# Performance work log

Hardware: AMD Instinct MI355X
Metric: run time of the kernel (lower is better)

## Reference

```python
import jax, jax.numpy as jnp
import numpy as np

B, D_IN, HD, HN = 16384, 1024, 128, 8
D = HD * HN  # 1024
PROJ = int((4.0 / 3.0) * D)  # 1365
EPS = 1e-5


def setup_inputs() -> dict:
    key = jax.random.key(0)
    ks = jax.random.split(key, 16)
    s = 0.02
    inp = {
        'seq': jax.random.normal(ks[0], (B, D_IN), jnp.float32),
        'c0': jnp.zeros((B, D), jnp.float32),
        'n0': jnp.ones((B, D), jnp.float32),
        'h0': jax.random.normal(ks[1], (B, D), jnp.float32) * 0.1,
        'm0': jnp.zeros((B, D), jnp.float32),
        'ln_w': jnp.ones((D_IN,), jnp.float32),
        'ln_b': jnp.zeros((D_IN,), jnp.float32),
        'Wz': jax.random.normal(ks[2], (D, D_IN), jnp.float32) * s,
        'bz': jnp.zeros((D,), jnp.float32),
        'Wi': jax.random.normal(ks[3], (D, D_IN), jnp.float32) * s,
        'bi': jnp.zeros((D,), jnp.float32),
        'Wo': jax.random.normal(ks[4], (D, D_IN), jnp.float32) * s,
        'bo': jnp.zeros((D,), jnp.float32),
        'Wf': jax.random.normal(ks[5], (D, D_IN), jnp.float32) * s,
        'bf': jnp.zeros((D,), jnp.float32),
        'Rz': jax.random.normal(ks[6], (HN, HD, HD), jnp.float32) * s,
        'Ri': jax.random.normal(ks[7], (HN, HD, HD), jnp.float32) * s,
        'Ro': jax.random.normal(ks[8], (HN, HD, HD), jnp.float32) * s,
        'Rf': jax.random.normal(ks[9], (HN, HD, HD), jnp.float32) * s,
        'gn_w': jnp.ones((D,), jnp.float32),
        'gn_b': jnp.zeros((D,), jnp.float32),
        'up_w': jax.random.normal(ks[10], (2 * PROJ, D), jnp.float32) * s,
        'up_b': jnp.zeros((2 * PROJ,), jnp.float32),
        'down_w': jax.random.normal(ks[11], (D_IN, PROJ), jnp.float32) * s,
        'down_b': jnp.zeros((D_IN,), jnp.float32),
    }
    return inp


def _layernorm(x, w, b):
    mu = jnp.mean(x, axis=-1, keepdims=True)
    var = jnp.mean(jnp.square(x - mu), axis=-1, keepdims=True)
    return (x - mu) * jax.lax.rsqrt(var + EPS) * w + b


def _groupnorm(x, w, b):
    # x: (B, D) -> groups of HD channels per head
    xr = x.reshape(x.shape[0], HN, HD)
    mu = jnp.mean(xr, axis=-1, keepdims=True)
    var = jnp.mean(jnp.square(xr - mu), axis=-1, keepdims=True)
    xn = ((xr - mu) * jax.lax.rsqrt(var + EPS)).reshape(x.shape)
    return xn * w + b


def _block_linear(h, R):
    # block-diagonal recurrence: per-head (HD,HD) matmul
    hr = h.reshape(h.shape[0], HN, HD)
    return jnp.einsum('hed,bhd->bhe', R, hr).reshape(h.shape)


def reference(seq, c0, n0, h0, m0, ln_w, ln_b, Wz, bz, Wi, bi, Wo, bo, Wf, bf,
              Rz, Ri, Ro, Rf, gn_w, gn_b, up_w, up_b, down_w, down_b):
    x_t = _layernorm(seq, ln_w, ln_b)
    x_c = x_t  # use_conv=False default path
    i_t = x_c @ Wi.T + bi + _block_linear(h0, Ri)
    f_t = x_c @ Wf.T + bf + _block_linear(h0, Rf)
    z_t = x_t @ Wz.T + bz + _block_linear(h0, Rz)
    o_t = x_t @ Wo.T + bo + _block_linear(h0, Ro)
    m_t = jnp.maximum(f_t + m0, i_t)
    i_e = jnp.exp(i_t - m_t)
    f_e = jnp.exp(f_t - m_t + m0)
    z_a = jnp.tanh(z_t)
    o_a = jax.nn.sigmoid(o_t)
    c_t = f_e * c0 + i_e * z_a
    n_t = f_e * n0 + i_e
    h_t = o_a * (c_t / n_t)
    out = _groupnorm(h_t, gn_w, gn_b)
    up = out @ up_w.T + up_b
    out1, out2 = jnp.split(up, 2, axis=-1)
    out = out1 + jax.nn.gelu(out2, approximate=False)
    out = out @ down_w.T + down_b
    return (out + seq, c_t, n_t, h_t, m_t)
```

## Files before the change

### kernel.cpp

```cpp
#include <hip/hip_runtime.h>
#include <hip/hip_bf16.h>
#include <cstdint>
#include <type_traits>

typedef __attribute__((ext_vector_type(8))) __bf16 bf16x8;
typedef __attribute__((ext_vector_type(8))) short short8;
typedef __attribute__((ext_vector_type(4))) float f32x4;
using u16 = unsigned short;

template <typename T, typename = void> struct mfma_ok : std::false_type {};
template <typename T>
struct mfma_ok<T, std::void_t<decltype(__builtin_amdgcn_mfma_f32_16x16x32_bf16(
    std::declval<T>(), std::declval<T>(), std::declval<f32x4>(), 0, 0, 0))>>
    : std::true_type {};
using frag_t = std::conditional_t<mfma_ok<bf16x8>::value, bf16x8, short8>;
static_assert(sizeof(frag_t) == 16, "frag must be 4 VGPRs");

template <typename T>
__device__ __forceinline__ f32x4 MFMA(T a, T b, f32x4 c) {
  return __builtin_amdgcn_mfma_f32_16x16x32_bf16(a, b, c, 0, 0, 0);
}

__device__ __forceinline__ void gl_lds16(const u16* g, u16* l) {
  __builtin_amdgcn_global_load_lds(
      (const __attribute__((address_space(1))) unsigned int*)g,
      (__attribute__((address_space(3))) unsigned int*)l, 16, 0, 0);
}

__device__ __forceinline__ u16 f2bf(float v) {
  __hip_bfloat16 h = __float2bfloat16(v);
  return __builtin_bit_cast(u16, h);
}

__device__ __forceinline__ int xcd_swz(int wid, int nwg) {
  return (wid & 7) * (nwg >> 3) + (wid >> 3);
}

__device__ __forceinline__ void gemm256(
    const u16* __restrict__ A, int lda,
    const u16* __restrict__ B, int ldb, int K,
    u16* lds, f32x4 (&acc)[8][4])
{
  const int t = threadIdx.x;
  const int l = t & 63;
  const int w = t >> 6;
  const int wm = w >> 2, wc = w & 3;

  const int sr = t >> 2;
  const int cs = (t & 3) ^ ((sr & 3) ^ ((sr >> 2) & 3));
  const u16* gA = A + sr * lda + cs * 8;
  const u16* gB = B + sr * ldb + cs * 8;

  const int lr = l & 15;
  const int kceff = (l >> 4) ^ ((l & 3) ^ ((l >> 2) & 3));
  const int abase = wm * 4096 + lr * 32 + kceff * 8;
  const int bbase = 8192 + wc * 2048 + lr * 32 + kceff * 8;

  const int nt = K >> 5;

#define STG(buf, kt) do {                                      \
    u16* s_ = (buf);                                           \
    const u16* a_ = gA + (kt) * 32;                            \
    const u16* b_ = gB + (kt) * 32;                            \
    gl_lds16(a_,             s_ + w * 512);                    \
    gl_lds16(a_ + 128 * lda, s_ +  4096 + w * 512);            \
    gl_lds16(b_,             s_ +  8192 + w * 512);            \
    gl_lds16(b_ + 128 * ldb, s_ + 12288 + w * 512);            \
  } while (0)

  STG(lds, 0);
  asm volatile("s_waitcnt vmcnt(0)" ::: "memory");
  __builtin_amdgcn_s_barrier();

  for (int kt = 0; kt < nt; ++kt) {
    u16* cur = lds + (kt & 1) * 16384;
    u16* nxt = lds + ((kt + 1) & 1) * 16384;
    const bool more = (kt + 1 < nt);
    if (more) STG(nxt, kt + 1);

    frag_t a[8], b[4];
#pragma unroll
    for (int fm = 0; fm < 8; ++fm)
      a[fm] = *(const frag_t*)(cur + abase + fm * 512);
#pragma unroll
    for (int fn = 0; fn < 4; ++fn)
      b[fn] = *(const frag_t*)(cur + bbase + fn * 512);

    __builtin_amdgcn_s_setprio(1);
#pragma unroll
    for (int fn = 0; fn < 4; ++fn)
#pragma unroll
      for (int fm = 0; fm < 8; ++fm)
        acc[fm][fn] = MFMA(a[fm], b[fn], acc[fm][fn]);
    __builtin_amdgcn_s_setprio(0);

    if (more) asm volatile("s_waitcnt vmcnt(0)" ::: "memory");
    else      asm volatile("" ::: "memory");
    __builtin_amdgcn_s_barrier();
  }
#undef STG
}

__global__ __launch_bounds__(256) void prep_kernel(
    const float* __restrict__ Wi, const float* __restrict__ Wf,
    const float* __restrict__ Wz, const float* __restrict__ Wo,
    const float* __restrict__ Ri, const float* __restrict__ Rf,
    const float* __restrict__ Rz, const float* __restrict__ Ro,
    const float* __restrict__ upw, const float* __restrict__ dnw,
    u16* __restrict__ Wint, u16* __restrict__ Rint,
    u16* __restrict__ upint, u16* __restrict__ dnp)
{
  const int stride = gridDim.x * 256;
  for (int i = blockIdx.x * 256 + threadIdx.x; i < 9043968; i += stride) {
    if (i < 4194304) {
      const int s = i >> 18, v = (i >> 10) & 255, k = i & 1023;
      const int wc = v >> 6, gsel = (v >> 4) & 3, c16 = v & 15;
      const int srcRow = s * 64 + wc * 16 + c16;
      const float* W = (gsel == 0) ? Wi : (gsel == 1) ? Wf : (gsel == 2) ? Wz : Wo;
      Wint[i] = f2bf(W[srcRow * 1024 + k]);
    } else if (i < 4718592) {
      const int j = i - 4194304;
      const int s = j >> 15, v = (j >> 7) & 255, k = j & 127;
      const int wc = v >> 6, gsel = (v >> 4) & 3, c16 = v & 15;
      const int head = s >> 1;
      const int colInHead = (s & 1) * 64 + wc * 16 + c16;
      const float* R = (gsel == 0) ? Ri : (gsel == 1) ? Rf : (gsel == 2) ? Rz : Ro;
      Rint[j] = f2bf(R[head * 16384 + colInHead * 128 + k]);
    } else if (i < 7602176) {
      const int j = i - 4718592;
      const int vcol = j >> 10, k = j & 1023;
      const int tile = vcol >> 8, wc = (vcol >> 6) & 3;
      const int half = (vcol >> 5) & 1, c32 = vcol & 31;
      const int a = tile * 128 + wc * 32 + c32;
      upint[j] = (a < 1365) ? f2bf(upw[(half * 1365 + a) * 1024 + k]) : (u16)0;
    } else {
      const int j = i - 7602176;
      const int row = j / 1408, k = j - row * 1408;
      dnp[j] = (k < 1365) ? f2bf(dnw[row * 1365 + k]) : (u16)0;
    }
  }
}

__global__ __launch_bounds__(256) void ln_kernel(
    const float* __restrict__ seq, const float* __restrict__ h0,
    const float* __restrict__ lnw, const float* __restrict__ lnb,
    u16* __restrict__ xb, u16* __restrict__ h0b)
{
  const int row = blockIdx.x;
  const int t = threadIdx.x;
  const float4 v = ((const float4*)(seq + (size_t)row * 1024))[t];
  float s = v.x + v.y + v.z + v.w;
  float q = v.x * v.x + v.y * v.y + v.z * v.z + v.w * v.w;
#pragma unroll
  for (int o = 32; o >= 1; o >>= 1) { s += __shfl_xor(s, o); q += __shfl_xor(q, o); }
  __shared__ float sm[8];
  const int l = t & 63, w = t >> 6;
  if (l == 0) { sm[w] = s; sm[4 + w] = q; }
  __syncthreads();
  s = sm[0] + sm[1] + sm[2] + sm[3];
  q = sm[4] + sm[5] + sm[6] + sm[7];
  const float mu = s * (1.f / 1024.f);
  const float var = q * (1.f / 1024.f) - mu * mu;
  const float rstd = rsqrtf(var + 1e-5f);
  const float4 wv = ((const float4*)lnw)[t];
  const float4 bv = ((const float4*)lnb)[t];
  ushort4 o4;
  o4.x = f2bf((v.x - mu) * rstd * wv.x + bv.x);
  o4.y = f2bf((v.y - mu) * rstd * wv.y + bv.y);
  o4.z = f2bf((v.z - mu) * rstd * wv.z + bv.z);
  o4.w = f2bf((v.w - mu) * rstd * wv.w + bv.w);
  ((ushort4*)(xb + (size_t)row * 1024))[t] = o4;
  const float4 h = ((const float4*)(h0 + (size_t)row * 1024))[t];
  ushort4 h4;
  h4.x = f2bf(h.x); h4.y = f2bf(h.y); h4.z = f2bf(h.z); h4.w = f2bf(h.w);
  ((ushort4*)(h0b + (size_t)row * 1024))[t] = h4;
}

__global__ __launch_bounds__(512, 2) void gate_kernel(
    const u16* __restrict__ xb, const u16* __restrict__ h0b,
    const u16* __restrict__ Wint, const u16* __restrict__ Rint,
    const float* __restrict__ bi, const float* __restrict__ bfv,
    const float* __restrict__ bz, const float* __restrict__ bo,
    const float* __restrict__ c0, const float* __restrict__ n0i,
    const float* __restrict__ m0,
    float* __restrict__ oc, float* __restrict__ on,
    float* __restrict__ oh, float* __restrict__ om)
{
  __shared__ __align__(16) u16 lds[32768];
  const int wid = xcd_swz(blockIdx.x, 1024);
  const int s = wid & 15;
  const int m0r = (wid >> 4) * 256;
  f32x4 acc[8][4] = {};
  gemm256(xb + (size_t)m0r * 1024, 1024, Wint + s * 262144, 1024, 1024, lds, acc);
  const int head = s >> 1;
  gemm256(h0b + (size_t)m0r * 1024 + head * 128, 1024,
          Rint + s * 32768, 128, 128, lds, acc);

  const int t = threadIdx.x, l = t & 63, w = t >> 6, wm = w >> 2, wc = w & 3;
  const int cc = s * 64 + wc * 16 + (l & 15);
  const float biv = bi[cc], bfvv = bfv[cc], bzv = bz[cc], bov = bo[cc];
#pragma unroll
  for (int fm = 0; fm < 8; ++fm) {
    const int rbase = m0r + wm * 128 + fm * 16 + (l >> 4) * 4;
#pragma unroll
    for (int r = 0; r < 4; ++r) {
      const size_t idx = (size_t)(rbase + r) * 1024 + cc;
      const float it = acc[fm][0][r] + biv;
      const float ft = acc[fm][1][r] + bfvv;
      const float zt = acc[fm][2][r] + bzv;
      const float ot = acc[fm][3][r] + bov;
      const float mp = m0[idx];
      const float mt = fmaxf(ft + mp, it);
      const float ie = __expf(it - mt);
      const float fe = __expf(ft - mt + mp);
      const float ct = fe * c0[idx] + ie * tanhf(zt);
      const float nt = fe * n0i[idx] + ie;
      const float ht = (ct / nt) / (1.f + __expf(-ot));
      oc[idx] = ct; on[idx] = nt; oh[idx] = ht; om[idx] = mt;
    }
  }
}

__global__ __launch_bounds__(256) void gn_kernel(
    const float* __restrict__ h, const float* __restrict__ gw,
    const float* __restrict__ gb, u16* __restrict__ gnb)
{
  const int t = threadIdx.x, l = t & 63, w = t >> 6;
  for (int grp = blockIdx.x * 4 + w; grp < 16384 * 8; grp += gridDim.x * 4) {
    const int b = grp >> 3, hd = grp & 7;
    const float2 v = ((const float2*)(h + b * 1024 + hd * 128))[l];
    float s = v.x + v.y, q = v.x * v.x + v.y * v.y;
#pragma unroll
    for (int o = 32; o >= 1; o >>= 1) { s += __shfl_xor(s, o); q += __shfl_xor(q, o); }
    const float mu = s * (1.f / 128.f);
    const float var = q * (1.f / 128.f) - mu * mu;
    const float rstd = rsqrtf(var + 1e-5f);
    const float2 wv = ((const float2*)(gw + hd * 128))[l];
    const float2 bv = ((const float2*)(gb + hd * 128))[l];
    ushort2 o2;
    o2.x = f2bf((v.x - mu) * rstd * wv.x + bv.x);
    o2.y = f2bf((v.y - mu) * rstd * wv.y + bv.y);
    ((ushort2*)(gnb + b * 1024 + hd * 128))[l] = o2;
  }
}

__global__ __launch_bounds__(512, 2) void up_kernel(
    const u16* __restrict__ gnb, const u16* __restrict__ upint,
    const float* __restrict__ upb, u16* __restrict__ g)
{
  __shared__ __align__(16) u16 lds[32768];
  const int wid = xcd_swz(blockIdx.x, 704);
  const int vt = wid % 11, mt = wid / 11;
  const int m0r = mt * 256;
  f32x4 acc[8][4] = {};
  gemm256(gnb + (size_t)m0r * 1024, 1024, upint + vt * 262144, 1024, 1024,
          lds, acc);
  const int t = threadIdx.x, l = t & 63, w = t >> 6, wm = w >> 2, wc = w & 3;
#pragma unroll
  for (int fm = 0; fm < 8; ++fm) {
    const int rbase = m0r + wm * 128 + fm * 16 + (l >> 4) * 4;
#pragma unroll
    for (int fn = 0; fn < 2; ++fn) {
      const int a = vt * 128 + wc * 32 + fn * 16 + (l & 15);
      const float b1 = (a < 1365) ? upb[a] : 0.f;
      const float b2 = (a < 1365) ? upb[1365 + a] : 0.f;
#pragma unroll
      for (int r = 0; r < 4; ++r) {
        const float u1 = acc[fm][fn][r] + b1;
        const float u2 = acc[fm][fn + 2][r] + b2;
        const float ge = 0.5f * u2 * (1.f + erff(u2 * 0.70710678118654752f));
        g[(size_t)(rbase + r) * 1408 + a] = f2bf(u1 + ge);
      }
    }
  }
}

__global__ __launch_bounds__(512, 2) void down_kernel(
    const u16* __restrict__ g, const u16* __restrict__ dnp,
    const float* __restrict__ dnb, const float* __restrict__ seq,
    float* __restrict__ out)
{
  __shared__ __align__(16) u16 lds[32768];
  const int wid = xcd_swz(blockIdx.x, 256);
  const int nc = (wid & 3) * 256;
  const int m0r = (wid >> 2) * 256;
  f32x4 acc[8][4] = {};
  gemm256(g + (size_t)m0r * 1408, 1408, dnp + nc * 1408, 1408, 1408, lds, acc);
  const int t = threadIdx.x, l = t & 63, w = t >> 6, wm = w >> 2, wc = w & 3;
#pragma unroll
  for (int fm = 0; fm < 8; ++fm) {
    const int rbase = m0r + wm * 128 + fm * 16 + (l >> 4) * 4;
#pragma unroll
    for (int fn = 0; fn < 4; ++fn) {
      const int cc = nc + wc * 64 + fn * 16 + (l & 15);
      const float bb = dnb[cc];
#pragma unroll
      for (int r = 0; r < 4; ++r) {
        const size_t idx = (size_t)(rbase + r) * 1024 + cc;
        out[idx] = acc[fm][fn][r] + bb + seq[idx];
      }
    }
  }
}

extern "C" void kernel_launch(void* const* d_in, const int* in_sizes, int n_in,
                              void* d_out, int out_size, void* d_ws, size_t ws_size,
                              hipStream_t stream) {
  const float* seq = (const float*)d_in[0];
  const float* c0  = (const float*)d_in[1];
  const float* n0i = (const float*)d_in[2];
  const float* h0  = (const float*)d_in[3];
  const float* m0  = (const float*)d_in[4];
  const float* lnw = (const float*)d_in[5];
  const float* lnb = (const float*)d_in[6];
  const float* Wz  = (const float*)d_in[7];
  const float* bz  = (const float*)d_in[8];
  const float* Wi  = (const float*)d_in[9];
  const float* bi  = (const float*)d_in[10];
  const float* Wo  = (const float*)d_in[11];
  const float* bo  = (const float*)d_in[12];
  const float* Wf  = (const float*)d_in[13];
  const float* bf_ = (const float*)d_in[14];
  const float* Rz  = (const float*)d_in[15];
  const float* Ri  = (const float*)d_in[16];
  const float* Ro  = (const float*)d_in[17];
  const float* Rf  = (const float*)d_in[18];
  const float* gw  = (const float*)d_in[19];
  const float* gb  = (const float*)d_in[20];
  const float* upw = (const float*)d_in[21];
  const float* upb = (const float*)d_in[22];
  const float* dnw = (const float*)d_in[23];
  const float* dnb = (const float*)d_in[24];

  char* ws = (char*)d_ws;
  u16* xb   = (u16*)(ws);
  u16* h0b  = (u16*)(ws + 33554432);
  u16* Wint = (u16*)(ws + 67108864);
  u16* Rint = (u16*)(ws + 75497472);
  u16* upc  = (u16*)(ws + 76546048);
  u16* dnp  = (u16*)(ws + 82313216);
  u16* g    = (u16*)(ws + 85196800);

  float* out = (float*)d_out;
  float* oc = out + 16777216;
  float* on = out + 2 * 16777216;
  float* oh = out + 3 * 16777216;
  float* om = out + 4 * 16777216;

  prep_kernel<<<dim3(2048), dim3(256), 0, stream>>>(
      Wi, Wf, Wz, Wo, Ri, Rf, Rz, Ro, upw, dnw, Wint, Rint, upc, dnp);
  ln_kernel<<<dim3(16384), dim3(256), 0, stream>>>(seq, h0, lnw, lnb, xb, h0b);
  gate_kernel<<<dim3(1024), dim3(512), 0, stream>>>(
      xb, h0b, Wint, Rint, bi, bf_, bz, bo, c0, n0i, m0, oc, on, oh, om);
  gn_kernel<<<dim3(2048), dim3(256), 0, stream>>>(oh, gw, gb, xb);
  up_kernel<<<dim3(704), dim3(512), 0, stream>>>(xb, upc, upb, g);
  down_kernel<<<dim3(256), dim3(512), 0, stream>>>(g, dnp, dnb, seq, out);
}
```

Before: 546.3 us.

## Switch GEMMs to 128x128 single-buffered tiles with smaller blocks

Replaces the 256x256 double-buffered, LDS-swizzled GEMM tile with a 128x128 tile run by 256-thread blocks, and repacks the gate and up weights to match. Grids grow fourfold so more blocks fill the CUs, especially for the down projection. In exchange the prefetch overlap and LDS swizzle are dropped, which exposes global-load latency and may add bank conflicts. Per-block data reuse is also lower.

```diff
diff --git a/kernel.cpp b/kernel.cpp
--- a/kernel.cpp
+++ b/kernel.cpp
@@ -36,69 +36,47 @@
   return (wid & 7) * (nwg >> 3) + (wid >> 3);
 }
 
-__device__ __forceinline__ void gemm256(
+__device__ __forceinline__ void gemm128(
     const u16* __restrict__ A, int lda,
     const u16* __restrict__ B, int ldb, int K,
-    u16* lds, f32x4 (&acc)[8][4])
+    u16* lds, f32x4 (&acc)[4][4])
 {
   const int t = threadIdx.x;
   const int l = t & 63;
   const int w = t >> 6;
-  const int wm = w >> 2, wc = w & 3;
-
-  const int sr = t >> 2;
-  const int cs = (t & 3) ^ ((sr & 3) ^ ((sr >> 2) & 3));
-  const u16* gA = A + sr * lda + cs * 8;
-  const u16* gB = B + sr * ldb + cs * 8;
-
-  const int lr = l & 15;
-  const int kceff = (l >> 4) ^ ((l & 3) ^ ((l >> 2) & 3));
-  const int abase = wm * 4096 + lr * 32 + kceff * 8;
-  const int bbase = 8192 + wc * 2048 + lr * 32 + kceff * 8;
+  const int wm = w >> 1, wc = w & 1;
+
+  const u16* gA = A + (t >> 2) * lda + (t & 3) * 8;
+  const u16* gB = B + (t >> 2) * ldb + (t & 3) * 8;
+
+  const int lr = l & 15, lk = l >> 4;
+  const int ab = (wm * 64 + lr) * 32 + lk * 8;
+  const int bb = 4096 + (wc * 64 + lr) * 32 + lk * 8;
 
   const int nt = K >> 5;
-
-#define STG(buf, kt) do {                                      \
-    u16* s_ = (buf);                                           \
-    const u16* a_ = gA + (kt) * 32;                            \
-    const u16* b_ = gB + (kt) * 32;                            \
-    gl_lds16(a_,             s_ + w * 512);                    \
-    gl_lds16(a_ + 128 * lda, s_ +  4096 + w * 512);            \
-    gl_lds16(b_,             s_ +  8192 + w * 512);            \
-    gl_lds16(b_ + 128 * ldb, s_ + 12288 + w * 512);            \
-  } while (0)
-
-  STG(lds, 0);
-  asm volatile("s_waitcnt vmcnt(0)" ::: "memory");
-  __builtin_amdgcn_s_barrier();
-
   for (int kt = 0; kt < nt; ++kt) {
-    u16* cur = lds + (kt & 1) * 16384;
-    u16* nxt = lds + ((kt + 1) & 1) * 16384;
-    const bool more = (kt + 1 < nt);
-    if (more) STG(nxt, kt + 1);
-
-    frag_t a[8], b[4];
-#pragma unroll
-    for (int fm = 0; fm < 8; ++fm)
-      a[fm] = *(const frag_t*)(cur + abase + fm * 512);
+    const u16* a_ = gA + kt * 32;
+    const u16* b_ = gB + kt * 32;
+    gl_lds16(a_,            lds + w * 512);
+    gl_lds16(a_ + 64 * lda, lds + 2048 + w * 512);
+    gl_lds16(b_,            lds + 4096 + w * 512);
+    gl_lds16(b_ + 64 * ldb, lds + 6144 + w * 512);
+    __syncthreads();
+
+    frag_t a[4], b[4];
+#pragma unroll
+    for (int fm = 0; fm < 4; ++fm)
+      a[fm] = *(const frag_t*)(lds + ab + fm * 512);
 #pragma unroll
     for (int fn = 0; fn < 4; ++fn)
-      b[fn] = *(const frag_t*)(cur + bbase + fn * 512);
-
-    __builtin_amdgcn_s_setprio(1);
+      b[fn] = *(const frag_t*)(lds + bb + fn * 512);
 #pragma unroll
     for (int fn = 0; fn < 4; ++fn)
 #pragma unroll
-      for (int fm = 0; fm < 8; ++fm)
+      for (int fm = 0; fm < 4; ++fm)
         acc[fm][fn] = MFMA(a[fm], b[fn], acc[fm][fn]);
-    __builtin_amdgcn_s_setprio(0);
-
-    if (more) asm volatile("s_waitcnt vmcnt(0)" ::: "memory");
-    else      asm volatile("" ::: "memory");
-    __builtin_amdgcn_s_barrier();
-  }
-#undef STG
+    __syncthreads();
+  }
 }
 
 __global__ __launch_bounds__(256) void prep_kernel(
@@ -113,25 +91,25 @@
   const int stride = gridDim.x * 256;
   for (int i = blockIdx.x * 256 + threadIdx.x; i < 9043968; i += stride) {
     if (i < 4194304) {
-      const int s = i >> 18, v = (i >> 10) & 255, k = i & 1023;
-      const int wc = v >> 6, gsel = (v >> 4) & 3, c16 = v & 15;
-      const int srcRow = s * 64 + wc * 16 + c16;
-      const float* W = (gsel == 0) ? Wi : (gsel == 1) ? Wf : (gsel == 2) ? Wz : Wo;
-      Wint[i] = f2bf(W[srcRow * 1024 + k]);
+      const int nt = i >> 17, vcol = (i >> 10) & 127, k = i & 1023;
+      const int wc = vcol >> 6, g = (vcol >> 4) & 3, c16 = vcol & 15;
+      const int col = nt * 32 + wc * 16 + c16;
+      const float* W = (g == 0) ? Wi : (g == 1) ? Wf : (g == 2) ? Wz : Wo;
+      Wint[i] = f2bf(W[col * 1024 + k]);
     } else if (i < 4718592) {
       const int j = i - 4194304;
-      const int s = j >> 15, v = (j >> 7) & 255, k = j & 127;
-      const int wc = v >> 6, gsel = (v >> 4) & 3, c16 = v & 15;
-      const int head = s >> 1;
-      const int colInHead = (s & 1) * 64 + wc * 16 + c16;
-      const float* R = (gsel == 0) ? Ri : (gsel == 1) ? Rf : (gsel == 2) ? Rz : Ro;
+      const int nt = j >> 14, vcol = (j >> 7) & 127, k = j & 127;
+      const int wc = vcol >> 6, g = (vcol >> 4) & 3, c16 = vcol & 15;
+      const int head = nt >> 2;
+      const int colInHead = (nt & 3) * 32 + wc * 16 + c16;
+      const float* R = (g == 0) ? Ri : (g == 1) ? Rf : (g == 2) ? Rz : Ro;
       Rint[j] = f2bf(R[head * 16384 + colInHead * 128 + k]);
     } else if (i < 7602176) {
       const int j = i - 4718592;
-      const int vcol = j >> 10, k = j & 1023;
-      const int tile = vcol >> 8, wc = (vcol >> 6) & 3;
-      const int half = (vcol >> 5) & 1, c32 = vcol & 31;
-      const int a = tile * 128 + wc * 32 + c32;
+      const int vt = j >> 17, vcol = (j >> 10) & 127, k = j & 1023;
+      const int wc = vcol >> 6, fn = (vcol >> 4) & 3, c16 = vcol & 15;
+      const int half = fn >> 1;
+      const int a = vt * 64 + wc * 32 + (fn & 1) * 16 + c16;
       upint[j] = (a < 1365) ? f2bf(upw[(half * 1365 + a) * 1024 + k]) : (u16)0;
     } else {
       const int j = i - 7602176;
@@ -176,7 +154,7 @@
   ((ushort4*)(h0b + (size_t)row * 1024))[t] = h4;
 }
 
-__global__ __launch_bounds__(512, 2) void gate_kernel(
+__global__ __launch_bounds__(256, 3) void gate_kernel(
     const u16* __restrict__ xb, const u16* __restrict__ h0b,
     const u16* __restrict__ Wint, const u16* __restrict__ Rint,
     const float* __restrict__ bi, const float* __restrict__ bfv,
@@ -186,22 +164,22 @@
     float* __restrict__ oc, float* __restrict__ on,
     float* __restrict__ oh, float* __restrict__ om)
 {
-  __shared__ __align__(16) u16 lds[32768];
-  const int wid = xcd_swz(blockIdx.x, 1024);
-  const int s = wid & 15;
-  const int m0r = (wid >> 4) * 256;
-  f32x4 acc[8][4] = {};
-  gemm256(xb + (size_t)m0r * 1024, 1024, Wint + s * 262144, 1024, 1024, lds, acc);
-  const int head = s >> 1;
-  gemm256(h0b + (size_t)m0r * 1024 + head * 128, 1024,
-          Rint + s * 32768, 128, 128, lds, acc);
-
-  const int t = threadIdx.x, l = t & 63, w = t >> 6, wm = w >> 2, wc = w & 3;
-  const int cc = s * 64 + wc * 16 + (l & 15);
+  __shared__ __align__(16) u16 lds[8192];
+  const int wid = xcd_swz(blockIdx.x, 4096);
+  const int nt = wid & 31;
+  const int mt = wid >> 5;
+  f32x4 acc[4][4] = {};
+  gemm128(xb + (size_t)mt * 131072, 1024, Wint + nt * 131072, 1024, 1024,
+          lds, acc);
+  gemm128(h0b + (size_t)mt * 131072 + (nt >> 2) * 128, 1024,
+          Rint + nt * 16384, 128, 128, lds, acc);
+
+  const int t = threadIdx.x, l = t & 63, w = t >> 6, wm = w >> 1, wc = w & 1;
+  const int cc = nt * 32 + wc * 16 + (l & 15);
   const float biv = bi[cc], bfvv = bfv[cc], bzv = bz[cc], bov = bo[cc];
 #pragma unroll
-  for (int fm = 0; fm < 8; ++fm) {
-    const int rbase = m0r + wm * 128 + fm * 16 + (l >> 4) * 4;
+  for (int fm = 0; fm < 4; ++fm) {
+    const int rbase = mt * 128 + wm * 64 + fm * 16 + (l >> 4) * 4;
 #pragma unroll
     for (int r = 0; r < 4; ++r) {
       const size_t idx = (size_t)(rbase + r) * 1024 + cc;
@@ -210,13 +188,13 @@
       const float zt = acc[fm][2][r] + bzv;
       const float ot = acc[fm][3][r] + bov;
       const float mp = m0[idx];
-      const float mt = fmaxf(ft + mp, it);
-      const float ie = __expf(it - mt);
-      const float fe = __expf(ft - mt + mp);
+      const float mt_ = fmaxf(ft + mp, it);
+      const float ie = __expf(it - mt_);
+      const float fe = __expf(ft - mt_ + mp);
       const float ct = fe * c0[idx] + ie * tanhf(zt);
-      const float nt = fe * n0i[idx] + ie;
-      const float ht = (ct / nt) / (1.f + __expf(-ot));
-      oc[idx] = ct; on[idx] = nt; oh[idx] = ht; om[idx] = mt;
+      const float ntv = fe * n0i[idx] + ie;
+      const float ht = (ct / ntv) / (1.f + __expf(-ot));
+      oc[idx] = ct; on[idx] = ntv; oh[idx] = ht; om[idx] = mt_;
     }
   }
 }
@@ -244,24 +222,23 @@
   }
 }
 
-__global__ __launch_bounds__(512, 2) void up_kernel(
+__global__ __launch_bounds__(256, 3) void up_kernel(
     const u16* __restrict__ gnb, const u16* __restrict__ upint,
     const float* __restrict__ upb, u16* __restrict__ g)
 {
-  __shared__ __align__(16) u16 lds[32768];
-  const int wid = xcd_swz(blockIdx.x, 704);
-  const int vt = wid % 11, mt = wid / 11;
-  const int m0r = mt * 256;
-  f32x4 acc[8][4] = {};
-  gemm256(gnb + (size_t)m0r * 1024, 1024, upint + vt * 262144, 1024, 1024,
+  __shared__ __align__(16) u16 lds[8192];
+  const int wid = xcd_swz(blockIdx.x, 2816);
+  const int vt = wid % 22, mt = wid / 22;
+  f32x4 acc[4][4] = {};
+  gemm128(gnb + (size_t)mt * 131072, 1024, upint + vt * 131072, 1024, 1024,
           lds, acc);
-  const int t = threadIdx.x, l = t & 63, w = t >> 6, wm = w >> 2, wc = w & 3;
-#pragma unroll
-  for (int fm = 0; fm < 8; ++fm) {
-    const int rbase = m0r + wm * 128 + fm * 16 + (l >> 4) * 4;
+  const int t = threadIdx.x, l = t & 63, w = t >> 6, wm = w >> 1, wc = w & 1;
+#pragma unroll
+  for (int fm = 0; fm < 4; ++fm) {
+    const int rbase = mt * 128 + wm * 64 + fm * 16 + (l >> 4) * 4;
 #pragma unroll
     for (int fn = 0; fn < 2; ++fn) {
-      const int a = vt * 128 + wc * 32 + fn * 16 + (l & 15);
+      const int a = vt * 64 + wc * 32 + fn * 16 + (l & 15);
       const float b1 = (a < 1365) ? upb[a] : 0.f;
       const float b2 = (a < 1365) ? upb[1365 + a] : 0.f;
 #pragma unroll
@@ -275,24 +252,24 @@
   }
 }
 
-__global__ __launch_bounds__(512, 2) void down_kernel(
+__global__ __launch_bounds__(256, 3) void down_kernel(
     const u16* __restrict__ g, const u16* __restrict__ dnp,
     const float* __restrict__ dnb, const float* __restrict__ seq,
     float* __restrict__ out)
 {
-  __shared__ __align__(16) u16 lds[32768];
-  const int wid = xcd_swz(blockIdx.x, 256);
-  const int nc = (wid & 3) * 256;
-  const int m0r = (wid >> 2) * 256;
-  f32x4 acc[8][4] = {};
-  gemm256(g + (size_t)m0r * 1408, 1408, dnp + nc * 1408, 1408, 1408, lds, acc);
-  const int t = threadIdx.x, l = t & 63, w = t >> 6, wm = w >> 2, wc = w & 3;
-#pragma unroll
-  for (int fm = 0; fm < 8; ++fm) {
-    const int rbase = m0r + wm * 128 + fm * 16 + (l >> 4) * 4;
+  __shared__ __align__(16) u16 lds[8192];
+  const int wid = xcd_swz(blockIdx.x, 1024);
+  const int nt = wid & 7, mt = wid >> 3;
+  f32x4 acc[4][4] = {};
+  gemm128(g + (size_t)mt * 180224, 1408, dnp + nt * 180224, 1408, 1408,
+          lds, acc);
+  const int t = threadIdx.x, l = t & 63, w = t >> 6, wm = w >> 1, wc = w & 1;
+#pragma unroll
+  for (int fm = 0; fm < 4; ++fm) {
+    const int rbase = mt * 128 + wm * 64 + fm * 16 + (l >> 4) * 4;
 #pragma unroll
     for (int fn = 0; fn < 4; ++fn) {
-      const int cc = nc + wc * 64 + fn * 16 + (l & 15);
+      const int cc = nt * 128 + wc * 64 + fn * 16 + (l & 15);
       const float bb = dnb[cc];
 #pragma unroll
       for (int r = 0; r < 4; ++r) {
@@ -350,9 +327,9 @@
   prep_kernel<<<dim3(2048), dim3(256), 0, stream>>>(
       Wi, Wf, Wz, Wo, Ri, Rf, Rz, Ro, upw, dnw, Wint, Rint, upc, dnp);
   ln_kernel<<<dim3(16384), dim3(256), 0, stream>>>(seq, h0, lnw, lnb, xb, h0b);
-  gate_kernel<<<dim3(1024), dim3(512), 0, stream>>>(
+  gate_kernel<<<dim3(4096), dim3(256), 0, stream>>>(
       xb, h0b, Wint, Rint, bi, bf_, bz, bo, c0, n0i, m0, oc, on, oh, om);
   gn_kernel<<<dim3(2048), dim3(256), 0, stream>>>(oh, gw, gb, xb);
-  up_kernel<<<dim3(704), dim3(512), 0, stream>>>(xb, upc, upb, g);
-  down_kernel<<<dim3(256), dim3(512), 0, stream>>>(g, dnp, dnb, seq, out);
-}
+  up_kernel<<<dim3(2816), dim3(256), 0, stream>>>(xb, upc, upb, g);
+  down_kernel<<<dim3(1024), dim3(256), 0, stream>>>(g, dnp, dnb, seq, out);
+}
```

New measurement: 563.9 us. +3.2%, slower.

## Deepen GEMM LDS pipeline to four-slot ring with prefetch distance two

Applied to the files above, without the earlier changes.

The shared bf16 GEMM loop moves from a two-buffer LDS scheme to a four-slot ring. It prefetches two K-steps ahead and waits with vmcnt(4) instead of draining all loads every iteration, to hide more global-to-LDS latency. The LDS bank swizzle is also changed to a simpler XOR on the row. Each block now needs twice the LDS, so gate, up and down kernels drop to one 512-thread block per CU. That halves resident waves, so there is less inter-block overlap to hide latency.

```diff
diff --git a/kernel.cpp b/kernel.cpp
--- a/kernel.cpp
+++ b/kernel.cpp
@@ -46,45 +46,43 @@
   const int w = t >> 6;
   const int wm = w >> 2, wc = w & 3;
 
-  const int sr = t >> 2;
-  const int cs = (t & 3) ^ ((sr & 3) ^ ((sr >> 2) & 3));
-  const u16* gA = A + sr * lda + cs * 8;
-  const u16* gB = B + sr * ldb + cs * 8;
-
-  const int lr = l & 15;
-  const int kceff = (l >> 4) ^ ((l & 3) ^ ((l >> 2) & 3));
-  const int abase = wm * 4096 + lr * 32 + kceff * 8;
-  const int bbase = 8192 + wc * 2048 + lr * 32 + kceff * 8;
-
-  const int nt = K >> 5;
-
-#define STG(buf, kt) do {                                      \
-    u16* s_ = (buf);                                           \
-    const u16* a_ = gA + (kt) * 32;                            \
-    const u16* b_ = gB + (kt) * 32;                            \
+  const int cs = (t & 3) ^ ((t >> 3) & 3);
+  const u16* gA = A + (t >> 2) * lda + cs * 8;
+  const u16* gB = B + (t >> 2) * ldb + cs * 8;
+
+  const int lr = l & 15, lk = l >> 4;
+  const int ck = (lk ^ ((lr >> 1) & 3)) * 8;
+  const int ab = (wm * 128 + lr) * 32 + ck;
+  const int bb = 8192 + (wc * 64 + lr) * 32 + ck;
+
+  const int ns = K >> 5;
+
+#define STG(s) do {                                            \
+    u16* s_ = lds + ((s) & 3) * 16384;                         \
+    const u16* a_ = gA + (s) * 32;                             \
+    const u16* b_ = gB + (s) * 32;                             \
     gl_lds16(a_,             s_ + w * 512);                    \
     gl_lds16(a_ + 128 * lda, s_ +  4096 + w * 512);            \
     gl_lds16(b_,             s_ +  8192 + w * 512);            \
     gl_lds16(b_ + 128 * ldb, s_ + 12288 + w * 512);            \
   } while (0)
 
-  STG(lds, 0);
-  asm volatile("s_waitcnt vmcnt(0)" ::: "memory");
+  STG(0);
+  STG(1);
+  asm volatile("s_waitcnt vmcnt(4)" ::: "memory");
   __builtin_amdgcn_s_barrier();
 
-  for (int kt = 0; kt < nt; ++kt) {
-    u16* cur = lds + (kt & 1) * 16384;
-    u16* nxt = lds + ((kt + 1) & 1) * 16384;
-    const bool more = (kt + 1 < nt);
-    if (more) STG(nxt, kt + 1);
+  for (int s = 0; s < ns; ++s) {
+    u16* cur = lds + (s & 3) * 16384;
+    if (s + 2 < ns) STG(s + 2);
 
     frag_t a[8], b[4];
 #pragma unroll
     for (int fm = 0; fm < 8; ++fm)
-      a[fm] = *(const frag_t*)(cur + abase + fm * 512);
+      a[fm] = *(const frag_t*)(cur + ab + fm * 512);
 #pragma unroll
     for (int fn = 0; fn < 4; ++fn)
-      b[fn] = *(const frag_t*)(cur + bbase + fn * 512);
+      b[fn] = *(const frag_t*)(cur + bb + fn * 512);
 
     __builtin_amdgcn_s_setprio(1);
 #pragma unroll
@@ -94,9 +92,11 @@
         acc[fm][fn] = MFMA(a[fm], b[fn], acc[fm][fn]);
     __builtin_amdgcn_s_setprio(0);
 
-    if (more) asm volatile("s_waitcnt vmcnt(0)" ::: "memory");
-    else      asm volatile("" ::: "memory");
-    __builtin_amdgcn_s_barrier();
+    if (s + 1 < ns) {
+      if (s + 2 < ns) asm volatile("s_waitcnt vmcnt(4)" ::: "memory");
+      else            asm volatile("s_waitcnt vmcnt(0)" ::: "memory");
+      __builtin_amdgcn_s_barrier();
+    }
   }
 #undef STG
 }
@@ -176,7 +176,7 @@
   ((ushort4*)(h0b + (size_t)row * 1024))[t] = h4;
 }
 
-__global__ __launch_bounds__(512, 2) void gate_kernel(
+__global__ __launch_bounds__(512, 1) void gate_kernel(
     const u16* __restrict__ xb, const u16* __restrict__ h0b,
     const u16* __restrict__ Wint, const u16* __restrict__ Rint,
     const float* __restrict__ bi, const float* __restrict__ bfv,
@@ -186,7 +186,7 @@
     float* __restrict__ oc, float* __restrict__ on,
     float* __restrict__ oh, float* __restrict__ om)
 {
-  __shared__ __align__(16) u16 lds[32768];
+  __shared__ __align__(16) u16 lds[65536];
   const int wid = xcd_swz(blockIdx.x, 1024);
   const int s = wid & 15;
   const int m0r = (wid >> 4) * 256;
@@ -244,11 +244,11 @@
   }
 }
 
-__global__ __launch_bounds__(512, 2) void up_kernel(
+__global__ __launch_bounds__(512, 1) void up_kernel(
     const u16* __restrict__ gnb, const u16* __restrict__ upint,
     const float* __restrict__ upb, u16* __restrict__ g)
 {
-  __shared__ __align__(16) u16 lds[32768];
+  __shared__ __align__(16) u16 lds[65536];
   const int wid = xcd_swz(blockIdx.x, 704);
   const int vt = wid % 11, mt = wid / 11;
   const int m0r = mt * 256;
@@ -275,12 +275,12 @@
   }
 }
 
-__global__ __launch_bounds__(512, 2) void down_kernel(
+__global__ __launch_bounds__(512, 1) void down_kernel(
     const u16* __restrict__ g, const u16* __restrict__ dnp,
     const float* __restrict__ dnb, const float* __restrict__ seq,
     float* __restrict__ out)
 {
-  __shared__ __align__(16) u16 lds[32768];
+  __shared__ __align__(16) u16 lds[65536];
   const int wid = xcd_swz(blockIdx.x, 256);
   const int nc = (wid & 3) * 256;
   const int m0r = (wid >> 2) * 256;
```

Measured after the change: 515.8 us. 5.6% less time.
